# Optimization experiments

Hardware: AMD Instinct MI355X
Metric: run time of the kernel (lower is better)

## Reference

```python
import jax, jax.numpy as jnp
import numpy as np

N, E, D_NLP, D_EMB = 100000, 500000, 768, 128


def setup_inputs() -> dict:
    key = jax.random.key(0)
    ks = jax.random.split(key, 6)
    z = jax.random.normal(ks[0], (N, D_EMB), jnp.float32)
    z0 = jax.random.normal(ks[1], (N, D_NLP), jnp.float32)
    edge_index = jax.random.randint(ks[2], (2, E), 0, N)
    w0 = jax.random.normal(ks[3], (D_EMB, D_NLP), jnp.float32) / np.sqrt(D_NLP)
    prelu_a = jnp.full((1,), 0.25, jnp.float32)  # torch PReLU default init
    w1 = jax.random.normal(ks[4], (1, 3 * D_EMB), jnp.float32) / np.sqrt(3 * D_EMB)
    b1 = jnp.zeros((1,), jnp.float32)
    return {"z": z, "z0": z0, "edge_index": edge_index, "w0": w0,
            "prelu_a": prelu_a, "w1": w1, "b1": b1}


def reference(z, z0, edge_index, w0, prelu_a, w1, b1):
    # qid = elementwise max of the two endpoint rows, shifted to start at 0
    qid = jnp.max(edge_index[0:2], axis=0)
    qid = qid - qid.min()
    # lin0 (no bias) + PReLU with scalar slope
    h = z0[qid] @ w0.T                       # [E, D_EMB]
    x0 = jnp.where(h >= 0, h, prelu_a[0] * h)
    emb1 = z[edge_index[0]]                  # [E, D_EMB]
    emb2 = z[edge_index[1]]                  # [E, D_EMB]
    # lin1(concat([emb1, emb2, x0])) == sum of three matvecs; avoids a [E, 3*D] concat
    w1a, w1b, w1c = w1[0, :D_EMB], w1[0, D_EMB:2 * D_EMB], w1[0, 2 * D_EMB:]
    out = emb1 @ w1a + emb2 @ w1b + x0 @ w1c + b1[0]
    return out  # [E]
```

## Files before the change

kernel.cpp:

```cpp
#include <hip/hip_runtime.h>
#include <hip/hip_bf16.h>
#include <stdint.h>

#define D_EMB 128
#define D_NLP 768
#define BM 64
#define BK 64
#define NKC (D_NLP / BK)

typedef __attribute__((ext_vector_type(8))) short bf16x8;
typedef __attribute__((ext_vector_type(4))) float f32x4;
typedef __attribute__((ext_vector_type(8))) unsigned short u16x8;

__device__ __forceinline__ unsigned short f2bf(float f) {
  unsigned u = __builtin_bit_cast(unsigned, f);
  u += 0x7fffu + ((u >> 16) & 1u);
  return (unsigned short)(u >> 16);
}

__device__ __forceinline__ bf16x8 pack8(const float4& a, const float4& b) {
  u16x8 v;
  v[0] = __builtin_bit_cast(unsigned short, __float2bfloat16(a.x));
  v[1] = __builtin_bit_cast(unsigned short, __float2bfloat16(a.y));
  v[2] = __builtin_bit_cast(unsigned short, __float2bfloat16(a.z));
  v[3] = __builtin_bit_cast(unsigned short, __float2bfloat16(a.w));
  v[4] = __builtin_bit_cast(unsigned short, __float2bfloat16(b.x));
  v[5] = __builtin_bit_cast(unsigned short, __float2bfloat16(b.y));
  v[6] = __builtin_bit_cast(unsigned short, __float2bfloat16(b.z));
  v[7] = __builtin_bit_cast(unsigned short, __float2bfloat16(b.w));
  return __builtin_bit_cast(bf16x8, v);
}

__global__ void kw(const float* __restrict__ w0, unsigned short* __restrict__ w0s,
                   int* __restrict__ mn) {
  if (blockIdx.x == 0 && threadIdx.x == 0) mn[0] = 0x7fffffff;
  int t = blockIdx.x * 256 + threadIdx.x;
  if (t >= (D_EMB * D_NLP) / 8) return;
  int u = t & 7, row = (t >> 3) & 127, kc = t >> 10;
  const float4* src = (const float4*)(w0 + (size_t)row * D_NLP + kc * 64 + ((u ^ (row & 7)) * 8));
  float4 v0 = src[0], v1 = src[1];
  u16x8 o;
  o[0] = f2bf(v0.x); o[1] = f2bf(v0.y); o[2] = f2bf(v0.z); o[3] = f2bf(v0.w);
  o[4] = f2bf(v1.x); o[5] = f2bf(v1.y); o[6] = f2bf(v1.z); o[7] = f2bf(v1.w);
  *(u16x8*)(w0s + (size_t)t * 8) = o;
}

__global__ void km(const int* __restrict__ ei, int E, int* __restrict__ mn) {
  int t = blockIdx.x * blockDim.x + threadIdx.x;
  int stride = gridDim.x * blockDim.x;
  int m = 0x7fffffff;
  for (int e = t; e < E; e += stride) {
    int a = ei[e], b = ei[E + e];
    int q = a > b ? a : b;
    m = q < m ? q : m;
  }
  #pragma unroll
  for (int off = 32; off; off >>= 1) {
    int o = __shfl_xor(m, off);
    m = o < m ? o : m;
  }
  if ((threadIdx.x & 63) == 0) atomicMin(mn, m);
}

__global__ __launch_bounds__(256) void kc(
    const float* __restrict__ z0, const float* __restrict__ z,
    const unsigned short* __restrict__ w0s, const float* __restrict__ w1,
    const float* __restrict__ prelu_a, float* __restrict__ sv,
    float* __restrict__ ta, float* __restrict__ tb, int N) {
  extern __shared__ char smem[];
  float* Al = (float*)smem;
  unsigned short* Bl = (unsigned short*)(smem + 49152);

  const int tid = threadIdx.x;
  const int lane = tid & 63;
  const int wave = tid >> 6;
  const int kg = lane >> 4;
  const int col = lane & 15;
  const int s16 = lane & 15;
  const int hl = lane >> 4;
  const int r0 = blockIdx.x * BM;
  const int myrow = r0 + wave * 16 + col;
  const int arow_g = min(myrow, N - 1);

  const float* aSrc[4];
  #pragma unroll
  for (int p = 0; p < 4; ++p) {
    int rl = p * 4 + hl;
    int rg = min(r0 + wave * 16 + rl, N - 1);
    int cu = s16 ^ (rl & 7);
    aSrc[p] = z0 + (size_t)rg * D_NLP + cu * 4;
  }

  auto stageA = [&](int t, int buf) {
    #pragma unroll
    for (int p = 0; p < 4; ++p) {
      __builtin_amdgcn_global_load_lds(
          (const __attribute__((address_space(1))) void*)(aSrc[p] + t * BK),
          (__attribute__((address_space(3))) void*)&Al[buf * 4096 + (wave * 16 + p * 4) * 64],
          16, 0, 0);
    }
  };

  auto stageB = [&](int t, int buf) {
    const unsigned short* g = w0s + (size_t)t * (D_EMB * BK) + (size_t)tid * 8;
    #pragma unroll
    for (int p = 0; p < 4; ++p) {
      __builtin_amdgcn_global_load_lds(
          (const __attribute__((address_space(1))) void*)(g + p * 256 * 8),
          (__attribute__((address_space(3))) void*)&Bl[buf * 8192 + (wave * 64 + p * 256) * 8],
          16, 0, 0);
    }
  };

  f32x4 acc[8];
  #pragma unroll
  for (int c = 0; c < 8; ++c) acc[c] = (f32x4){0.f, 0.f, 0.f, 0.f};

  stageB(0, 0);
  stageA(0, 0);
  stageA(1, 1);

  const int arow_l = (wave * 16 + col) * 64;
  const int asw = col & 7;

  #pragma unroll
  for (int t = 0; t < NKC; ++t) {
    if (t < NKC - 1) asm volatile("s_waitcnt vmcnt(4)" ::: "memory");
    else             asm volatile("s_waitcnt vmcnt(0)" ::: "memory");
    __builtin_amdgcn_s_barrier();
    if (t + 1 < NKC) stageB(t + 1, (t + 1) & 1);
    if (t + 2 < NKC) stageA(t + 2, (t + 2) % 3);
    __builtin_amdgcn_sched_barrier(0);

    const float* Ab = Al + (t % 3) * 4096;
    const unsigned short* Bbuf = Bl + (t & 1) * 8192;
    #pragma unroll
    for (int ks = 0; ks < 2; ++ks) {
      int u0 = ks * 8 + kg * 2;
      float4 lo = *(const float4*)&Ab[arow_l + ((u0)     ^ asw) * 4];
      float4 hi = *(const float4*)&Ab[arow_l + ((u0 + 1) ^ asw) * 4];
      bf16x8 af = pack8(lo, hi);
      #pragma unroll
      for (int c = 0; c < 8; ++c) {
        int brow = c * 16 + col;
        bf16x8 bfr = *(const bf16x8*)&Bbuf[(brow * 8 + ((ks * 4 + kg) ^ (brow & 7))) * 8];
        acc[c] = __builtin_amdgcn_mfma_f32_16x16x32_bf16(af, bfr, acc[c], 0, 0, 0);
      }
    }
  }

  float ap = prelu_a[0];
  float ssum[4] = {0.f, 0.f, 0.f, 0.f};
  #pragma unroll
  for (int c = 0; c < 8; ++c) {
    float wc = w1[2 * D_EMB + c * 16 + col];
    #pragma unroll
    for (int i = 0; i < 4; ++i) {
      float h = acc[c][i];
      float x = h >= 0.f ? h : ap * h;
      ssum[i] += x * wc;
    }
  }
  #pragma unroll
  for (int off = 1; off < 16; off <<= 1) {
    #pragma unroll
    for (int i = 0; i < 4; ++i) ssum[i] += __shfl_xor(ssum[i], off);
  }
  if (col == 0) {
    int rbase = r0 + wave * 16 + kg * 4;
    #pragma unroll
    for (int i = 0; i < 4; ++i) {
      int r = rbase + i;
      if (r < N) sv[r] = ssum[i];
    }
  }

  {
    const float* zp = z + (size_t)arow_g * D_EMB + kg * 32;
    const float4* wa4 = (const float4*)(w1 + kg * 32);
    const float4* wb4 = (const float4*)(w1 + D_EMB + kg * 32);
    float pa = 0.f, pb = 0.f;
    #pragma unroll
    for (int i = 0; i < 8; ++i) {
      float4 zv = ((const float4*)zp)[i];
      float4 wa = wa4[i];
      float4 wb = wb4[i];
      pa += zv.x * wa.x + zv.y * wa.y + zv.z * wa.z + zv.w * wa.w;
      pb += zv.x * wb.x + zv.y * wb.y + zv.z * wb.z + zv.w * wb.w;
    }
    pa += __shfl_xor(pa, 16); pa += __shfl_xor(pa, 32);
    pb += __shfl_xor(pb, 16); pb += __shfl_xor(pb, 32);
    if (kg == 0 && myrow < N) { ta[myrow] = pa; tb[myrow] = pb; }
  }
}

__global__ void kd(const int* __restrict__ ei, const int* __restrict__ mn,
                   const float* __restrict__ ta, const float* __restrict__ tb,
                   const float* __restrict__ sv, const float* __restrict__ b1,
                   float* __restrict__ out, int E) {
  int e = blockIdx.x * blockDim.x + threadIdx.x;
  if (e >= E) return;
  int i0 = ei[e], i1 = ei[E + e];
  int q = (i0 > i1 ? i0 : i1) - mn[0];
  out[e] = ta[i0] + tb[i1] + sv[q] + b1[0];
}

extern "C" void kernel_launch(void* const* d_in, const int* in_sizes, int n_in,
                              void* d_out, int out_size, void* d_ws, size_t ws_size,
                              hipStream_t stream) {
  const float* z  = (const float*)d_in[0];
  const float* z0 = (const float*)d_in[1];
  const int*   ei = (const int*)d_in[2];
  const float* w0 = (const float*)d_in[3];
  const float* pa = (const float*)d_in[4];
  const float* w1 = (const float*)d_in[5];
  const float* b1 = (const float*)d_in[6];
  float* out = (float*)d_out;
  const int N = in_sizes[0] / D_EMB;
  const int E = in_sizes[2] / 2;

  char* ws = (char*)d_ws;
  int* mn = (int*)ws;
  unsigned short* w0s = (unsigned short*)(ws + 256);
  float* ta = (float*)(ws + 256 + 196608);
  float* tb = ta + N;
  float* sv = tb + N;

  hipFuncSetAttribute((const void*)kc,
                      hipFuncAttributeMaxDynamicSharedMemorySize, 81920);

  kw<<<(D_EMB * D_NLP / 8 + 255) / 256, 256, 0, stream>>>(w0, w0s, mn);
  km<<<256, 256, 0, stream>>>(ei, E, mn);
  kc<<<(N + BM - 1) / BM, 256, 81920, stream>>>(z0, z, w0s, w1, pa, sv, ta, tb, N);
  kd<<<(E + 255) / 256, 256, 0, stream>>>(ei, mn, ta, tb, sv, b1, out, E);
}
```

Baseline: 120.4 us.

## Make GEMM kernel persistent and prefetch next tile during last k-step

The dense z0·w0 kernel becomes persistent with a fixed grid of 512 blocks that loop over row tiles. During the final k-chunk of each tile, the first stages of the next tile's A/B loads are issued so the epilogue and the tile switch overlap with memory traffic. The z row loads are also issued early into registers, and the w1 slice is hoisted out of the tile loop. This removes per-block launch and pipeline ramp-up costs. The trade-off is less parallelism per CU, since 512 blocks with 80KB of LDS each cap occupancy, and more register pressure from the extra live values.

Result: slower. 152.5 us (+26.7%).

```diff
diff --git a/kernel.cpp b/kernel.cpp
--- a/kernel.cpp
+++ b/kernel.cpp
@@ -7,6 +7,7 @@
 #define BM 64
 #define BK 64
 #define NKC (D_NLP / BK)
+#define NB 512
 
 typedef __attribute__((ext_vector_type(8))) short bf16x8;
 typedef __attribute__((ext_vector_type(4))) float f32x4;
@@ -66,7 +67,7 @@
     const float* __restrict__ z0, const float* __restrict__ z,
     const unsigned short* __restrict__ w0s, const float* __restrict__ w1,
     const float* __restrict__ prelu_a, float* __restrict__ sv,
-    float* __restrict__ ta, float* __restrict__ tb, int N) {
+    float* __restrict__ ta, float* __restrict__ tb, int N, int NT) {
   extern __shared__ char smem[];
   float* Al = (float*)smem;
   unsigned short* Bl = (unsigned short*)(smem + 49152);
@@ -78,29 +79,27 @@
   const int col = lane & 15;
   const int s16 = lane & 15;
   const int hl = lane >> 4;
-  const int r0 = blockIdx.x * BM;
-  const int myrow = r0 + wave * 16 + col;
-  const int arow_g = min(myrow, N - 1);
-
-  const float* aSrc[4];
-  #pragma unroll
-  for (int p = 0; p < 4; ++p) {
-    int rl = p * 4 + hl;
-    int rg = min(r0 + wave * 16 + rl, N - 1);
-    int cu = s16 ^ (rl & 7);
-    aSrc[p] = z0 + (size_t)rg * D_NLP + cu * 4;
-  }
-
-  auto stageA = [&](int t, int buf) {
+  const int arow_l = (wave * 16 + col) * 64;
+  const int asw = col & 7;
+
+  auto mkSrc = [&](int tile, const float* (&dst)[4]) {
+    int r0 = tile * BM;
+    #pragma unroll
+    for (int p = 0; p < 4; ++p) {
+      int rl = p * 4 + hl;
+      int rg = min(r0 + wave * 16 + rl, N - 1);
+      dst[p] = z0 + (size_t)rg * D_NLP + (s16 ^ (rl & 7)) * 4;
+    }
+  };
+  auto stageA = [&](const float* const (&src)[4], int t, int buf) {
     #pragma unroll
     for (int p = 0; p < 4; ++p) {
       __builtin_amdgcn_global_load_lds(
-          (const __attribute__((address_space(1))) void*)(aSrc[p] + t * BK),
+          (const __attribute__((address_space(1))) void*)(src[p] + t * BK),
           (__attribute__((address_space(3))) void*)&Al[buf * 4096 + (wave * 16 + p * 4) * 64],
           16, 0, 0);
     }
   };
-
   auto stageB = [&](int t, int buf) {
     const unsigned short* g = w0s + (size_t)t * (D_EMB * BK) + (size_t)tid * 8;
     #pragma unroll
@@ -116,81 +115,108 @@
   #pragma unroll
   for (int c = 0; c < 8; ++c) acc[c] = (f32x4){0.f, 0.f, 0.f, 0.f};
 
+  const float ap = prelu_a[0];
+  float wcf[8];
+  #pragma unroll
+  for (int c = 0; c < 8; ++c) wcf[c] = w1[2 * D_EMB + c * 16 + col];
+
+  const float* aSrc[4];
+  mkSrc(blockIdx.x, aSrc);
   stageB(0, 0);
-  stageA(0, 0);
-  stageA(1, 1);
-
-  const int arow_l = (wave * 16 + col) * 64;
-  const int asw = col & 7;
-
-  #pragma unroll
-  for (int t = 0; t < NKC; ++t) {
-    if (t < NKC - 1) asm volatile("s_waitcnt vmcnt(4)" ::: "memory");
-    else             asm volatile("s_waitcnt vmcnt(0)" ::: "memory");
-    __builtin_amdgcn_s_barrier();
-    if (t + 1 < NKC) stageB(t + 1, (t + 1) & 1);
-    if (t + 2 < NKC) stageA(t + 2, (t + 2) % 3);
-    __builtin_amdgcn_sched_barrier(0);
-
-    const float* Ab = Al + (t % 3) * 4096;
-    const unsigned short* Bbuf = Bl + (t & 1) * 8192;
-    #pragma unroll
-    for (int ks = 0; ks < 2; ++ks) {
-      int u0 = ks * 8 + kg * 2;
-      float4 lo = *(const float4*)&Ab[arow_l + ((u0)     ^ asw) * 4];
-      float4 hi = *(const float4*)&Ab[arow_l + ((u0 + 1) ^ asw) * 4];
-      bf16x8 af = pack8(lo, hi);
-      #pragma unroll
-      for (int c = 0; c < 8; ++c) {
-        int brow = c * 16 + col;
-        bf16x8 bfr = *(const bf16x8*)&Bbuf[(brow * 8 + ((ks * 4 + kg) ^ (brow & 7))) * 8];
-        acc[c] = __builtin_amdgcn_mfma_f32_16x16x32_bf16(af, bfr, acc[c], 0, 0, 0);
-      }
-    }
-  }
-
-  float ap = prelu_a[0];
-  float ssum[4] = {0.f, 0.f, 0.f, 0.f};
-  #pragma unroll
-  for (int c = 0; c < 8; ++c) {
-    float wc = w1[2 * D_EMB + c * 16 + col];
-    #pragma unroll
-    for (int i = 0; i < 4; ++i) {
-      float h = acc[c][i];
-      float x = h >= 0.f ? h : ap * h;
-      ssum[i] += x * wc;
-    }
-  }
-  #pragma unroll
-  for (int off = 1; off < 16; off <<= 1) {
-    #pragma unroll
-    for (int i = 0; i < 4; ++i) ssum[i] += __shfl_xor(ssum[i], off);
-  }
-  if (col == 0) {
-    int rbase = r0 + wave * 16 + kg * 4;
-    #pragma unroll
-    for (int i = 0; i < 4; ++i) {
-      int r = rbase + i;
-      if (r < N) sv[r] = ssum[i];
-    }
-  }
-
-  {
-    const float* zp = z + (size_t)arow_g * D_EMB + kg * 32;
-    const float4* wa4 = (const float4*)(w1 + kg * 32);
-    const float4* wb4 = (const float4*)(w1 + D_EMB + kg * 32);
-    float pa = 0.f, pb = 0.f;
-    #pragma unroll
-    for (int i = 0; i < 8; ++i) {
-      float4 zv = ((const float4*)zp)[i];
-      float4 wa = wa4[i];
-      float4 wb = wb4[i];
-      pa += zv.x * wa.x + zv.y * wa.y + zv.z * wa.z + zv.w * wa.w;
-      pb += zv.x * wb.x + zv.y * wb.y + zv.z * wb.z + zv.w * wb.w;
-    }
-    pa += __shfl_xor(pa, 16); pa += __shfl_xor(pa, 32);
-    pb += __shfl_xor(pb, 16); pb += __shfl_xor(pb, 32);
-    if (kg == 0 && myrow < N) { ta[myrow] = pa; tb[myrow] = pb; }
+  stageA(aSrc, 0, 0);
+  stageA(aSrc, 1, 1);
+
+  for (int tile = blockIdx.x; tile < NT; tile += NB) {
+    const int r0 = tile * BM;
+    const int myrow = r0 + wave * 16 + col;
+    const int arow_g = min(myrow, N - 1);
+    const bool hasNext = tile + NB < NT;
+    const float* aSrcN[4];
+    mkSrc(tile + NB, aSrcN);
+
+    float4 zr[8];
+
+    #pragma unroll
+    for (int t = 0; t < NKC; ++t) {
+      if (t < NKC - 1) asm volatile("s_waitcnt vmcnt(4)" ::: "memory");
+      else             asm volatile("s_waitcnt vmcnt(0)" ::: "memory");
+      __builtin_amdgcn_s_barrier();
+      if (t == NKC - 1) {
+        const float4* zp = (const float4*)(z + (size_t)arow_g * D_EMB + kg * 32);
+        #pragma unroll
+        for (int i = 0; i < 8; ++i) zr[i] = zp[i];
+        if (hasNext) {
+          stageB(0, 0);
+          stageA(aSrcN, 0, 0);
+          stageA(aSrcN, 1, 1);
+        }
+      } else {
+        stageB(t + 1, (t + 1) & 1);
+        if (t + 2 < NKC) stageA(aSrc, t + 2, (t + 2) % 3);
+      }
+      __builtin_amdgcn_sched_barrier(0);
+
+      const float* Ab = Al + (t % 3) * 4096;
+      const unsigned short* Bbuf = Bl + (t & 1) * 8192;
+      #pragma unroll
+      for (int ks = 0; ks < 2; ++ks) {
+        int u0 = ks * 8 + kg * 2;
+        float4 lo = *(const float4*)&Ab[arow_l + ((u0)     ^ asw) * 4];
+        float4 hi = *(const float4*)&Ab[arow_l + ((u0 + 1) ^ asw) * 4];
+        bf16x8 af = pack8(lo, hi);
+        #pragma unroll
+        for (int c = 0; c < 8; ++c) {
+          int brow = c * 16 + col;
+          bf16x8 bfr = *(const bf16x8*)&Bbuf[(brow * 8 + ((ks * 4 + kg) ^ (brow & 7))) * 8];
+          acc[c] = __builtin_amdgcn_mfma_f32_16x16x32_bf16(af, bfr, acc[c], 0, 0, 0);
+        }
+      }
+    }
+    #pragma unroll
+    for (int p = 0; p < 4; ++p) aSrc[p] = aSrcN[p];
+
+    float ssum[4] = {0.f, 0.f, 0.f, 0.f};
+    #pragma unroll
+    for (int c = 0; c < 8; ++c) {
+      #pragma unroll
+      for (int i = 0; i < 4; ++i) {
+        float h = acc[c][i];
+        float x = h >= 0.f ? h : ap * h;
+        ssum[i] += x * wcf[c];
+      }
+    }
+    #pragma unroll
+    for (int off = 1; off < 16; off <<= 1) {
+      #pragma unroll
+      for (int i = 0; i < 4; ++i) ssum[i] += __shfl_xor(ssum[i], off);
+    }
+    if (col == 0) {
+      int rbase = r0 + wave * 16 + kg * 4;
+      #pragma unroll
+      for (int i = 0; i < 4; ++i) {
+        int r = rbase + i;
+        if (r < N) sv[r] = ssum[i];
+      }
+    }
+    #pragma unroll
+    for (int c = 0; c < 8; ++c) acc[c] = (f32x4){0.f, 0.f, 0.f, 0.f};
+
+    {
+      const float4* wa4 = (const float4*)(w1 + kg * 32);
+      const float4* wb4 = (const float4*)(w1 + D_EMB + kg * 32);
+      float pa = 0.f, pb = 0.f;
+      #pragma unroll
+      for (int i = 0; i < 8; ++i) {
+        float4 zv = zr[i];
+        float4 wa = wa4[i];
+        float4 wb = wb4[i];
+        pa += zv.x * wa.x + zv.y * wa.y + zv.z * wa.z + zv.w * wa.w;
+        pb += zv.x * wb.x + zv.y * wb.y + zv.z * wb.z + zv.w * wb.w;
+      }
+      pa += __shfl_xor(pa, 16); pa += __shfl_xor(pa, 32);
+      pb += __shfl_xor(pb, 16); pb += __shfl_xor(pb, 32);
+      if (kg == 0 && myrow < N) { ta[myrow] = pa; tb[myrow] = pb; }
+    }
   }
 }
 
@@ -218,6 +244,7 @@
   float* out = (float*)d_out;
   const int N = in_sizes[0] / D_EMB;
   const int E = in_sizes[2] / 2;
+  const int NT = (N + BM - 1) / BM;
 
   char* ws = (char*)d_ws;
   int* mn = (int*)ws;
@@ -231,6 +258,6 @@
 
   kw<<<(D_EMB * D_NLP / 8 + 255) / 256, 256, 0, stream>>>(w0, w0s, mn);
   km<<<256, 256, 0, stream>>>(ei, E, mn);
-  kc<<<(N + BM - 1) / BM, 256, 81920, stream>>>(z0, z, w0s, w1, pa, sv, ta, tb, N);
+  kc<<<(NT < NB ? NT : NB), 256, 81920, stream>>>(z0, z, w0s, w1, pa, sv, ta, tb, N, NT);
   kd<<<(E + 255) / 256, 256, 0, stream>>>(ei, mn, ta, tb, sv, b1, out, E);
 }
```

## Shrink row tile to 16 and split output columns across waves

Applied to the files above, without the earlier changes.

The GEMM kernel now processes 16 z0 rows per block instead of 64, with each of the four waves computing a 32-column slice of the 128 outputs. Partial PReLU-dot sums are combined across waves through LDS. The K loop is hand-unrolled with a three-stage B buffer and A loaded in 256-wide chunks, double buffered. This gives four times as many blocks for better occupancy and latency hiding, but each block re-reads the whole w0 weight matrix, so weight traffic from L2 rises fourfold and there is an extra reduction step.

New measurement: 159.5 us. +32.5%, slower.

```diff
diff --git a/kernel.cpp b/kernel.cpp
--- a/kernel.cpp
+++ b/kernel.cpp
@@ -4,9 +4,8 @@
 
 #define D_EMB 128
 #define D_NLP 768
-#define BM 64
-#define BK 64
-#define NKC (D_NLP / BK)
+#define TR 16
+#define NKC 12
 
 typedef __attribute__((ext_vector_type(8))) short bf16x8;
 typedef __attribute__((ext_vector_type(4))) float f32x4;
@@ -69,40 +68,35 @@
     float* __restrict__ ta, float* __restrict__ tb, int N) {
   extern __shared__ char smem[];
   float* Al = (float*)smem;
-  unsigned short* Bl = (unsigned short*)(smem + 49152);
+  unsigned short* Bl = (unsigned short*)(smem + 32768);
 
   const int tid = threadIdx.x;
   const int lane = tid & 63;
   const int wave = tid >> 6;
   const int kg = lane >> 4;
   const int col = lane & 15;
-  const int s16 = lane & 15;
-  const int hl = lane >> 4;
-  const int r0 = blockIdx.x * BM;
-  const int myrow = r0 + wave * 16 + col;
-  const int arow_g = min(myrow, N - 1);
+  const int asw = col & 7;
+  const int r0 = blockIdx.x * TR;
 
   const float* aSrc[4];
   #pragma unroll
   for (int p = 0; p < 4; ++p) {
-    int rl = p * 4 + hl;
-    int rg = min(r0 + wave * 16 + rl, N - 1);
-    int cu = s16 ^ (rl & 7);
-    aSrc[p] = z0 + (size_t)rg * D_NLP + cu * 4;
-  }
-
-  auto stageA = [&](int t, int buf) {
+    int rl = wave * 4 + p;
+    int rg = min(r0 + rl, N - 1);
+    aSrc[p] = z0 + (size_t)rg * D_NLP + ((lane ^ (rl & 7)) * 4);
+  }
+
+  auto stageA = [&](int g, int buf) {
     #pragma unroll
     for (int p = 0; p < 4; ++p) {
       __builtin_amdgcn_global_load_lds(
-          (const __attribute__((address_space(1))) void*)(aSrc[p] + t * BK),
-          (__attribute__((address_space(3))) void*)&Al[buf * 4096 + (wave * 16 + p * 4) * 64],
+          (const __attribute__((address_space(1))) void*)(aSrc[p] + g * 256),
+          (__attribute__((address_space(3))) void*)&Al[buf * 4096 + (wave * 4 + p) * 256],
           16, 0, 0);
     }
   };
-
   auto stageB = [&](int t, int buf) {
-    const unsigned short* g = w0s + (size_t)t * (D_EMB * BK) + (size_t)tid * 8;
+    const unsigned short* g = w0s + (size_t)t * (D_EMB * 64) + (size_t)tid * 8;
     #pragma unroll
     for (int p = 0; p < 4; ++p) {
       __builtin_amdgcn_global_load_lds(
@@ -112,51 +106,51 @@
     }
   };
 
-  f32x4 acc[8];
-  #pragma unroll
-  for (int c = 0; c < 8; ++c) acc[c] = (f32x4){0.f, 0.f, 0.f, 0.f};
-
+  f32x4 acc[2];
+  acc[0] = (f32x4){0.f, 0.f, 0.f, 0.f};
+  acc[1] = (f32x4){0.f, 0.f, 0.f, 0.f};
+
+  stageA(0, 0);
   stageB(0, 0);
-  stageA(0, 0);
   stageA(1, 1);
-
-  const int arow_l = (wave * 16 + col) * 64;
-  const int asw = col & 7;
-
-  #pragma unroll
-  for (int t = 0; t < NKC; ++t) {
-    if (t < NKC - 1) asm volatile("s_waitcnt vmcnt(4)" ::: "memory");
-    else             asm volatile("s_waitcnt vmcnt(0)" ::: "memory");
-    __builtin_amdgcn_s_barrier();
-    if (t + 1 < NKC) stageB(t + 1, (t + 1) & 1);
-    if (t + 2 < NKC) stageA(t + 2, (t + 2) % 3);
-    __builtin_amdgcn_sched_barrier(0);
-
-    const float* Ab = Al + (t % 3) * 4096;
-    const unsigned short* Bbuf = Bl + (t & 1) * 8192;
-    #pragma unroll
-    for (int ks = 0; ks < 2; ++ks) {
-      int u0 = ks * 8 + kg * 2;
-      float4 lo = *(const float4*)&Ab[arow_l + ((u0)     ^ asw) * 4];
-      float4 hi = *(const float4*)&Ab[arow_l + ((u0 + 1) ^ asw) * 4];
-      bf16x8 af = pack8(lo, hi);
-      #pragma unroll
-      for (int c = 0; c < 8; ++c) {
-        int brow = c * 16 + col;
-        bf16x8 bfr = *(const bf16x8*)&Bbuf[(brow * 8 + ((ks * 4 + kg) ^ (brow & 7))) * 8];
-        acc[c] = __builtin_amdgcn_mfma_f32_16x16x32_bf16(af, bfr, acc[c], 0, 0, 0);
-      }
-    }
-  }
+  stageB(1, 1);
+
+#define KITER(T, VM) do {                                                     \
+    asm volatile("s_waitcnt vmcnt(" #VM ")" ::: "memory");                    \
+    __builtin_amdgcn_s_barrier();                                             \
+    if ((T) + 2 < NKC) stageB((T) + 2, ((T) + 2) % 3);                        \
+    if ((T) == 4) stageA(2, 0);                                               \
+    __builtin_amdgcn_sched_barrier(0);                                        \
+    const float* Ab = Al + (((T) >> 2) & 1) * 4096;                           \
+    const unsigned short* Bbuf = Bl + ((T) % 3) * 8192;                       \
+    _Pragma("unroll")                                                         \
+    for (int ks = 0; ks < 2; ++ks) {                                          \
+      int u0 = ((T) & 3) * 16 + ks * 8 + kg * 2;                              \
+      float4 lo = *(const float4*)&Ab[col * 256 + ((u0)     ^ asw) * 4];      \
+      float4 hi = *(const float4*)&Ab[col * 256 + ((u0 + 1) ^ asw) * 4];      \
+      bf16x8 af = pack8(lo, hi);                                              \
+      _Pragma("unroll")                                                       \
+      for (int bc = 0; bc < 2; ++bc) {                                        \
+        int brow = wave * 32 + bc * 16 + col;                                 \
+        bf16x8 bfr = *(const bf16x8*)&Bbuf[(brow * 8 + ((ks * 4 + kg) ^ (brow & 7))) * 8]; \
+        acc[bc] = __builtin_amdgcn_mfma_f32_16x16x32_bf16(af, bfr, acc[bc], 0, 0, 0); \
+      }                                                                       \
+    }                                                                         \
+  } while (0)
+
+  KITER(0, 8);  KITER(1, 4);  KITER(2, 4);  KITER(3, 4);
+  KITER(4, 4);  KITER(5, 8);  KITER(6, 8);  KITER(7, 4);
+  KITER(8, 4);  KITER(9, 4);  KITER(10, 4); KITER(11, 0);
+#undef KITER
 
   float ap = prelu_a[0];
   float ssum[4] = {0.f, 0.f, 0.f, 0.f};
   #pragma unroll
-  for (int c = 0; c < 8; ++c) {
-    float wc = w1[2 * D_EMB + c * 16 + col];
+  for (int bc = 0; bc < 2; ++bc) {
+    float wc = w1[2 * D_EMB + wave * 32 + bc * 16 + col];
     #pragma unroll
     for (int i = 0; i < 4; ++i) {
-      float h = acc[c][i];
+      float h = acc[bc][i];
       float x = h >= 0.f ? h : ap * h;
       ssum[i] += x * wc;
     }
@@ -166,31 +160,36 @@
     #pragma unroll
     for (int i = 0; i < 4; ++i) ssum[i] += __shfl_xor(ssum[i], off);
   }
+  __syncthreads();
+  float* red = Al;
   if (col == 0) {
-    int rbase = r0 + wave * 16 + kg * 4;
-    #pragma unroll
-    for (int i = 0; i < 4; ++i) {
-      int r = rbase + i;
-      if (r < N) sv[r] = ssum[i];
-    }
+    #pragma unroll
+    for (int i = 0; i < 4; ++i) red[wave * 16 + kg * 4 + i] = ssum[i];
+  }
+  __syncthreads();
+  if (tid < TR) {
+    int r = r0 + tid;
+    if (r < N) sv[r] = red[tid] + red[16 + tid] + red[32 + tid] + red[48 + tid];
   }
 
   {
-    const float* zp = z + (size_t)arow_g * D_EMB + kg * 32;
-    const float4* wa4 = (const float4*)(w1 + kg * 32);
-    const float4* wb4 = (const float4*)(w1 + D_EMB + kg * 32);
-    float pa = 0.f, pb = 0.f;
-    #pragma unroll
-    for (int i = 0; i < 8; ++i) {
-      float4 zv = ((const float4*)zp)[i];
-      float4 wa = wa4[i];
-      float4 wb = wb4[i];
-      pa += zv.x * wa.x + zv.y * wa.y + zv.z * wa.z + zv.w * wa.w;
-      pb += zv.x * wb.x + zv.y * wb.y + zv.z * wb.z + zv.w * wb.w;
-    }
-    pa += __shfl_xor(pa, 16); pa += __shfl_xor(pa, 32);
-    pb += __shfl_xor(pb, 16); pb += __shfl_xor(pb, 32);
-    if (kg == 0 && myrow < N) { ta[myrow] = pa; tb[myrow] = pb; }
+    int zr = r0 + wave * 4 + kg;
+    int rg = min(zr, N - 1);
+    const float4* zp = (const float4*)(z + (size_t)rg * D_EMB + col * 8);
+    float4 z0v = zp[0], z1v = zp[1];
+    const float4* wa4 = (const float4*)(w1 + col * 8);
+    const float4* wb4 = (const float4*)(w1 + D_EMB + col * 8);
+    float4 wa0 = wa4[0], wa1 = wa4[1];
+    float4 wb0 = wb4[0], wb1 = wb4[1];
+    float pa = z0v.x * wa0.x + z0v.y * wa0.y + z0v.z * wa0.z + z0v.w * wa0.w
+             + z1v.x * wa1.x + z1v.y * wa1.y + z1v.z * wa1.z + z1v.w * wa1.w;
+    float pb = z0v.x * wb0.x + z0v.y * wb0.y + z0v.z * wb0.z + z0v.w * wb0.w
+             + z1v.x * wb1.x + z1v.y * wb1.y + z1v.z * wb1.z + z1v.w * wb1.w;
+    pa += __shfl_xor(pa, 1); pb += __shfl_xor(pb, 1);
+    pa += __shfl_xor(pa, 2); pb += __shfl_xor(pb, 2);
+    pa += __shfl_xor(pa, 4); pb += __shfl_xor(pb, 4);
+    pa += __shfl_xor(pa, 8); pb += __shfl_xor(pb, 8);
+    if (col == 0 && zr < N) { ta[zr] = pa; tb[zr] = pb; }
   }
 }
 
@@ -231,6 +230,6 @@
 
   kw<<<(D_EMB * D_NLP / 8 + 255) / 256, 256, 0, stream>>>(w0, w0s, mn);
   km<<<256, 256, 0, stream>>>(ei, E, mn);
-  kc<<<(N + BM - 1) / BM, 256, 81920, stream>>>(z0, z, w0s, w1, pa, sv, ta, tb, N);
+  kc<<<(N + TR - 1) / TR, 256, 81920, stream>>>(z0, z, w0s, w1, pa, sv, ta, tb, N);
   kd<<<(E + 255) / 256, 256, 0, stream>>>(ei, mn, ta, tb, sv, b1, out, E);
 }
```

## Pre-convert z0 to swizzled bf16 tiles before the GEMM kernel

Applied to the files above, without the earlier changes.

Adds a kernel that converts z0 from fp32 to bf16 and writes it into a tiled, swizzled layout in workspace. The GEMM then streams half-size A tiles and skips the in-loop conversion. This costs an extra full read of fp32 z0 plus a write and re-read of the bf16 copy. It falls back to the old kernel when the workspace is too small.

New measurement: 163.9 us. 1.36x slower.

```diff
diff --git a/kernel.cpp b/kernel.cpp
--- a/kernel.cpp
+++ b/kernel.cpp
@@ -7,6 +7,7 @@
 #define BM 64
 #define BK 64
 #define NKC (D_NLP / BK)
+#define TUNITS 6144
 
 typedef __attribute__((ext_vector_type(8))) short bf16x8;
 typedef __attribute__((ext_vector_type(4))) float f32x4;
@@ -18,17 +19,14 @@
   return (unsigned short)(u >> 16);
 }
 
+__device__ __forceinline__ u16x8 pack8u(const float4& a, const float4& b) {
+  u16x8 v;
+  v[0] = f2bf(a.x); v[1] = f2bf(a.y); v[2] = f2bf(a.z); v[3] = f2bf(a.w);
+  v[4] = f2bf(b.x); v[5] = f2bf(b.y); v[6] = f2bf(b.z); v[7] = f2bf(b.w);
+  return v;
+}
 __device__ __forceinline__ bf16x8 pack8(const float4& a, const float4& b) {
-  u16x8 v;
-  v[0] = __builtin_bit_cast(unsigned short, __float2bfloat16(a.x));
-  v[1] = __builtin_bit_cast(unsigned short, __float2bfloat16(a.y));
-  v[2] = __builtin_bit_cast(unsigned short, __float2bfloat16(a.z));
-  v[3] = __builtin_bit_cast(unsigned short, __float2bfloat16(a.w));
-  v[4] = __builtin_bit_cast(unsigned short, __float2bfloat16(b.x));
-  v[5] = __builtin_bit_cast(unsigned short, __float2bfloat16(b.y));
-  v[6] = __builtin_bit_cast(unsigned short, __float2bfloat16(b.z));
-  v[7] = __builtin_bit_cast(unsigned short, __float2bfloat16(b.w));
-  return __builtin_bit_cast(bf16x8, v);
+  return __builtin_bit_cast(bf16x8, pack8u(a, b));
 }
 
 __global__ void kw(const float* __restrict__ w0, unsigned short* __restrict__ w0s,
@@ -38,11 +36,7 @@
   if (t >= (D_EMB * D_NLP) / 8) return;
   int u = t & 7, row = (t >> 3) & 127, kc = t >> 10;
   const float4* src = (const float4*)(w0 + (size_t)row * D_NLP + kc * 64 + ((u ^ (row & 7)) * 8));
-  float4 v0 = src[0], v1 = src[1];
-  u16x8 o;
-  o[0] = f2bf(v0.x); o[1] = f2bf(v0.y); o[2] = f2bf(v0.z); o[3] = f2bf(v0.w);
-  o[4] = f2bf(v1.x); o[5] = f2bf(v1.y); o[6] = f2bf(v1.z); o[7] = f2bf(v1.w);
-  *(u16x8*)(w0s + (size_t)t * 8) = o;
+  *(u16x8*)(w0s + (size_t)t * 8) = pack8u(src[0], src[1]);
 }
 
 __global__ void km(const int* __restrict__ ei, int E, int* __restrict__ mn) {
@@ -62,7 +56,141 @@
   if ((threadIdx.x & 63) == 0) atomicMin(mn, m);
 }
 
-__global__ __launch_bounds__(256) void kc(
+__global__ void kz(const float* __restrict__ z0, unsigned short* __restrict__ zt,
+                   int N, int units_total) {
+  int g = blockIdx.x * 256 + threadIdx.x;
+  if (g >= units_total) return;
+  unsigned rg = (unsigned)g / 96u;
+  int u = g - (int)rg * 96;
+  int srow = min((int)rg, N - 1);
+  const float4* s = (const float4*)(z0 + (size_t)srow * D_NLP + u * 8);
+  float4 a = s[0], b = s[1];
+  int T = rg >> 6, r = rg & 63, c = u >> 3, j = u & 7;
+  size_t dst = (size_t)T * TUNITS + c * 512 + r * 8 + (j ^ (r & 7));
+  *(u16x8*)(zt + dst * 8) = pack8u(a, b);
+}
+
+__global__ __launch_bounds__(256) void kc2(
+    const unsigned short* __restrict__ zt, const float* __restrict__ z,
+    const unsigned short* __restrict__ w0s, const float* __restrict__ w1,
+    const float* __restrict__ prelu_a, float* __restrict__ sv,
+    float* __restrict__ ta, float* __restrict__ tb, int N) {
+  __shared__ unsigned short Al[3][512 * 8];
+  __shared__ unsigned short Bl[2][8192];
+
+  const int tid = threadIdx.x;
+  const int lane = tid & 63;
+  const int wave = tid >> 6;
+  const int kg = lane >> 4;
+  const int col = lane & 15;
+  const int r0 = blockIdx.x * BM;
+  const int myrow = r0 + wave * 16 + col;
+  const int arow_g = min(myrow, N - 1);
+  const size_t abase = (size_t)blockIdx.x * TUNITS;
+
+  auto stageA = [&](int t, int buf) {
+    const unsigned short* g =
+        zt + (abase + (size_t)t * 512 + (size_t)(wave * 128 + lane)) * 8;
+    #pragma unroll
+    for (int i = 0; i < 2; ++i) {
+      __builtin_amdgcn_global_load_lds(
+          (const __attribute__((address_space(1))) void*)(g + i * 64 * 8),
+          (__attribute__((address_space(3))) void*)&Al[buf][(wave * 128 + i * 64) * 8],
+          16, 0, 0);
+    }
+  };
+  auto stageB = [&](int t, int buf) {
+    const unsigned short* g = w0s + (size_t)t * (D_EMB * BK) + (size_t)tid * 8;
+    #pragma unroll
+    for (int p = 0; p < 4; ++p) {
+      __builtin_amdgcn_global_load_lds(
+          (const __attribute__((address_space(1))) void*)(g + p * 256 * 8),
+          (__attribute__((address_space(3))) void*)&Bl[buf][(wave * 64 + p * 256) * 8],
+          16, 0, 0);
+    }
+  };
+
+  f32x4 acc[8];
+  #pragma unroll
+  for (int c = 0; c < 8; ++c) acc[c] = (f32x4){0.f, 0.f, 0.f, 0.f};
+
+  stageB(0, 0);
+  stageA(0, 0);
+  stageA(1, 1);
+
+  const int arw = (wave * 16 + col) * 8;
+  const int asw = col & 7;
+
+  #pragma unroll
+  for (int t = 0; t < NKC; ++t) {
+    if (t < NKC - 1) asm volatile("s_waitcnt vmcnt(2)" ::: "memory");
+    else             asm volatile("s_waitcnt vmcnt(0)" ::: "memory");
+    __builtin_amdgcn_s_barrier();
+    if (t + 1 < NKC) stageB(t + 1, (t + 1) & 1);
+    if (t + 2 < NKC) stageA(t + 2, (t + 2) % 3);
+    __builtin_amdgcn_sched_barrier(0);
+
+    const unsigned short* Ab = Al[t % 3];
+    const unsigned short* Bbuf = Bl[t & 1];
+    #pragma unroll
+    for (int ks = 0; ks < 2; ++ks) {
+      bf16x8 af = *(const bf16x8*)&Ab[(arw + ((ks * 4 + kg) ^ asw)) * 8];
+      #pragma unroll
+      for (int c = 0; c < 8; ++c) {
+        int brow = c * 16 + col;
+        bf16x8 bfr = *(const bf16x8*)&Bl[t & 1][(brow * 8 + ((ks * 4 + kg) ^ (brow & 7))) * 8];
+        acc[c] = __builtin_amdgcn_mfma_f32_16x16x32_bf16(af, bfr, acc[c], 0, 0, 0);
+      }
+      (void)Bbuf;
+    }
+  }
+
+  float ap = prelu_a[0];
+  float ssum[4] = {0.f, 0.f, 0.f, 0.f};
+  #pragma unroll
+  for (int c = 0; c < 8; ++c) {
+    float wc = w1[2 * D_EMB + c * 16 + col];
+    #pragma unroll
+    for (int i = 0; i < 4; ++i) {
+      float h = acc[c][i];
+      float x = h >= 0.f ? h : ap * h;
+      ssum[i] += x * wc;
+    }
+  }
+  #pragma unroll
+  for (int off = 1; off < 16; off <<= 1) {
+    #pragma unroll
+    for (int i = 0; i < 4; ++i) ssum[i] += __shfl_xor(ssum[i], off);
+  }
+  if (col == 0) {
+    int rbase = r0 + wave * 16 + kg * 4;
+    #pragma unroll
+    for (int i = 0; i < 4; ++i) {
+      int r = rbase + i;
+      if (r < N) sv[r] = ssum[i];
+    }
+  }
+
+  {
+    const float* zp = z + (size_t)arow_g * D_EMB + kg * 32;
+    const float4* wa4 = (const float4*)(w1 + kg * 32);
+    const float4* wb4 = (const float4*)(w1 + D_EMB + kg * 32);
+    float pa = 0.f, pb = 0.f;
+    #pragma unroll
+    for (int i = 0; i < 8; ++i) {
+      float4 zv = ((const float4*)zp)[i];
+      float4 wa = wa4[i];
+      float4 wb = wb4[i];
+      pa += zv.x * wa.x + zv.y * wa.y + zv.z * wa.z + zv.w * wa.w;
+      pb += zv.x * wb.x + zv.y * wb.y + zv.z * wb.z + zv.w * wb.w;
+    }
+    pa += __shfl_xor(pa, 16); pa += __shfl_xor(pa, 32);
+    pb += __shfl_xor(pb, 16); pb += __shfl_xor(pb, 32);
+    if (kg == 0 && myrow < N) { ta[myrow] = pa; tb[myrow] = pb; }
+  }
+}
+
+__global__ __launch_bounds__(256) void kc1(
     const float* __restrict__ z0, const float* __restrict__ z,
     const unsigned short* __restrict__ w0s, const float* __restrict__ w1,
     const float* __restrict__ prelu_a, float* __restrict__ sv,
@@ -100,7 +228,6 @@
           16, 0, 0);
     }
   };
-
   auto stageB = [&](int t, int buf) {
     const unsigned short* g = w0s + (size_t)t * (D_EMB * BK) + (size_t)tid * 8;
     #pragma unroll
@@ -174,7 +301,6 @@
       if (r < N) sv[r] = ssum[i];
     }
   }
-
   {
     const float* zp = z + (size_t)arow_g * D_EMB + kg * 32;
     const float4* wa4 = (const float4*)(w1 + kg * 32);
@@ -218,6 +344,7 @@
   float* out = (float*)d_out;
   const int N = in_sizes[0] / D_EMB;
   const int E = in_sizes[2] / 2;
+  const int NT = (N + BM - 1) / BM;
 
   char* ws = (char*)d_ws;
   int* mn = (int*)ws;
@@ -225,12 +352,21 @@
   float* ta = (float*)(ws + 256 + 196608);
   float* tb = ta + N;
   float* sv = tb + N;
-
-  hipFuncSetAttribute((const void*)kc,
-                      hipFuncAttributeMaxDynamicSharedMemorySize, 81920);
+  const size_t zt_off = (size_t)4 << 20;
+  unsigned short* zt = (unsigned short*)(ws + zt_off);
+  const size_t need = zt_off + (size_t)NT * TUNITS * 16;
+  const bool big = ws_size >= need;
 
   kw<<<(D_EMB * D_NLP / 8 + 255) / 256, 256, 0, stream>>>(w0, w0s, mn);
   km<<<256, 256, 0, stream>>>(ei, E, mn);
-  kc<<<(N + BM - 1) / BM, 256, 81920, stream>>>(z0, z, w0s, w1, pa, sv, ta, tb, N);
+  if (big) {
+    const int units = NT * BM * (D_NLP / 8);
+    kz<<<(units + 255) / 256, 256, 0, stream>>>(z0, zt, N, units);
+    kc2<<<NT, 256, 0, stream>>>(zt, z, w0s, w1, pa, sv, ta, tb, N);
+  } else {
+    hipFuncSetAttribute((const void*)kc1,
+                        hipFuncAttributeMaxDynamicSharedMemorySize, 81920);
+    kc1<<<NT, 256, 81920, stream>>>(z0, z, w0s, w1, pa, sv, ta, tb, N);
+  }
   kd<<<(E + 255) / 256, 256, 0, stream>>>(ei, mn, ta, tb, sv, b1, out, E);
 }
```
